# Kernel tuning notes

Measured on AMD Instinct MI355X. Metric: run time of the kernel, lower is better.

The kernel has to match this reference:

```python
import jax, jax.numpy as jnp
import numpy as np


def setup_inputs() -> dict:
    key = jax.random.key(0)
    kx, kw = jax.random.split(key)
    x = jax.random.normal(kx, (32, 256, 56, 56), dtype=jnp.float32)
    weight = jax.random.uniform(kw, (256, 256, 3, 3), dtype=jnp.float32) * 0.001
    return {"x": x, "weight": weight}


def reference(x, weight):
    # --- binarize activations with straight-through estimator ---
    # forward value = sign(x); gradient flows through clamp(x, -1, 1)
    clipped_x = jnp.clip(x, -1.0, 1.0)
    bx = jax.lax.stop_gradient(jnp.sign(x) - clipped_x) + clipped_x

    # --- binarize weights (per-output-channel mean-centered, scaled sign) ---
    w = weight
    # subtract per-output-channel mean over (in_c, kh, kw)
    bw = w - jnp.mean(w.reshape(w.shape[0], -1), axis=-1)[:, None, None, None]
    # per-output-channel scaling factor = mean |bw| (detached)
    scale = jnp.mean(jnp.abs(bw), axis=(1, 2, 3), keepdims=True)
    scale = jax.lax.stop_gradient(scale)
    clipped_w = jnp.clip(bw, -1.0, 1.0)
    binary_w = jax.lax.stop_gradient(scale * jnp.sign(bw) - clipped_w) + clipped_w

    # --- conv2d, NCHW / OIHW, stride 1, padding 1 ---
    y = jax.lax.conv_general_dilated(
        bx, binary_w,
        window_strides=(1, 1),
        padding=((1, 1), (1, 1)),
        dimension_numbers=("NCHW", "OIHW", "NCHW"),
    )
    return y
```

## Files before the change

### kernel.cpp

```cpp
#include <hip/hip_runtime.h>
#include <cstdint>
#include <cstddef>

#define N_ 32
#define C_ 256
#define H_ 56
#define W_ 56

typedef int v4i __attribute__((ext_vector_type(4)));

static constexpr size_t SX_BYTES = (size_t)N_ * 58 * 68 * 256;
static constexpr size_t WB_OFF   = SX_BYTES;
static constexpr size_t WB_BYTES = 36ull * 16 * 64 * 16;
static constexpr size_t SC_OFF   = WB_OFF + WB_BYTES;

__global__ __launch_bounds__(256) void zero_sx(v4i* __restrict__ p) {
    size_t i = (size_t)blockIdx.x * 256 + threadIdx.x;
    v4i z = {0, 0, 0, 0};
    p[i] = z;
}

__global__ __launch_bounds__(256) void pack_x(const float* __restrict__ x,
                                              char* __restrict__ sx) {
    __shared__ float tile[64 * 65];
    int tid = threadIdx.x;
    int hw0 = blockIdx.x * 64;
    int cb0 = blockIdx.y;
    int n   = blockIdx.z;

    int cl = tid >> 6, hwl = tid & 63;
    const float* xb = x + ((size_t)n * C_ + cb0 * 64) * 3136 + hw0;
#pragma unroll
    for (int i = 0; i < 16; ++i) {
        int cloc = i * 4 + cl;
        tile[cloc * 65 + hwl] = xb[(size_t)cloc * 3136 + hwl];
    }
    __syncthreads();

    int hwl2 = tid >> 2, cq = tid & 3;
    int hw = hw0 + hwl2;
    int h = hw / 56, w = hw - h * 56;
    int words[4];
#pragma unroll
    for (int g = 0; g < 4; ++g) {
        int word = 0;
#pragma unroll
        for (int b = 0; b < 4; ++b) {
            float v = tile[(cq * 16 + g * 4 + b) * 65 + hwl2];
            int s = (v > 0.0f) - (v < 0.0f);
            word |= (s & 0xff) << (8 * b);
        }
        words[g] = word;
    }
    v4i o4 = {words[0], words[1], words[2], words[3]};
    *(v4i*)(sx + (((size_t)n * 58 + h + 1) * 68 + (w + 1)) * 256 + cb0 * 64 + cq * 16) = o4;
}

__global__ __launch_bounds__(256) void pack_w(const float* __restrict__ wt,
                                              char* __restrict__ wB,
                                              float* __restrict__ scaleg) {
    __shared__ double red[256];
    int o = blockIdx.x, tid = threadIdx.x;
    const float* wo = wt + (size_t)o * 2304;

    double s = 0;
    for (int j = tid; j < 2304; j += 256) s += (double)wo[j];
    red[tid] = s;
    __syncthreads();
    for (int k = 128; k > 0; k >>= 1) {
        if (tid < k) red[tid] += red[tid + k];
        __syncthreads();
    }
    double mean = red[0] / 2304.0;
    __syncthreads();

    double s2 = 0;
    for (int j = tid; j < 2304; j += 256) s2 += fabs((double)wo[j] - mean);
    red[tid] = s2;
    __syncthreads();
    for (int k = 128; k > 0; k >>= 1) {
        if (tid < k) red[tid] += red[tid + k];
        __syncthreads();
    }
    if (tid == 0) scaleg[o] = (float)(red[0] / 2304.0);

    if (tid < 144) {
        int kiter = tid >> 2, q = tid & 3;
        int tap = kiter >> 2, cb = kiter & 3;
        int kh = tap / 3, kw = tap - kh * 3;
        int words[4];
        for (int g = 0; g < 4; ++g) {
            int word = 0;
            for (int b = 0; b < 4; ++b) {
                int c = cb * 64 + q * 16 + g * 4 + b;
                double v = (double)wo[c * 9 + kh * 3 + kw];
                int sg = (v > mean) - (v < mean);
                word |= (sg & 0xff) << (8 * b);
            }
            words[g] = word;
        }
        v4i pk = {words[0], words[1], words[2], words[3]};
        *(v4i*)(wB + (((size_t)kiter * 16 + (o >> 4)) * 64 + q * 16 + (o & 15)) * 16) = pk;
    }
}

__global__ __launch_bounds__(256, 3) void conv_mfma(const char* __restrict__ sx,
                                                    const v4i* __restrict__ wB,
                                                    const float* __restrict__ scaleg,
                                                    float* __restrict__ out) {
    __shared__ char xs[3 * 68 * 256];
    int tid = threadIdx.x;
    int wave = tid >> 6, lane = tid & 63;
    int h = blockIdx.x, n = blockIdx.y;

    const char* src = sx + ((size_t)n * 58 + h) * (68 * 256);
    for (int i = tid; i < 3 * 68 * 16; i += 256) {
        int w = (i >> 4) % 68;
        v4i v = *(const v4i*)(src + (size_t)i * 16);
        int phys = (i & ~15) | ((i + w) & 15);
        *(v4i*)(xs + (size_t)phys * 16) = v;
    }
    __syncthreads();

    int lm = lane & 15, q = lane >> 4;
    v4i acc[4][4];
#pragma unroll
    for (int mf = 0; mf < 4; ++mf)
#pragma unroll
        for (int of = 0; of < 4; ++of) {
            v4i z = {0, 0, 0, 0};
            acc[mf][of] = z;
        }

    for (int dh = 0; dh < 3; ++dh)
        for (int dw = 0; dw < 3; ++dw)
            for (int cb = 0; cb < 4; ++cb) {
                int kiter = (dh * 3 + dw) * 4 + cb;
                v4i b[4];
#pragma unroll
                for (int of = 0; of < 4; ++of)
                    b[of] = wB[((size_t)kiter * 16 + wave * 4 + of) * 64 + lane];
                v4i a[4];
#pragma unroll
                for (int mf = 0; mf < 4; ++mf) {
                    int win = mf * 16 + lm + dw;
                    int phys = ((dh * 68 + win) << 4) | ((cb * 4 + q + win) & 15);
                    a[mf] = *(const v4i*)(xs + (size_t)phys * 16);
                }
#pragma unroll
                for (int mf = 0; mf < 4; ++mf)
#pragma unroll
                    for (int of = 0; of < 4; ++of)
                        acc[mf][of] = __builtin_amdgcn_mfma_i32_16x16x64_i8(
                            a[mf], b[of], acc[mf][of], 0, 0, 0);
            }

#pragma unroll
    for (int of = 0; of < 4; ++of) {
        int o = (wave * 4 + of) * 16 + lm;
        float s = scaleg[o];
        float* ob = out + ((size_t)(n * C_ + o) * H_ + h) * W_;
#pragma unroll
        for (int mf = 0; mf < 4; ++mf) {
            int wb = mf * 16 + q * 4;
            if (wb < W_) {
                float4 v = {s * (float)acc[mf][of].x, s * (float)acc[mf][of].y,
                            s * (float)acc[mf][of].z, s * (float)acc[mf][of].w};
                *(float4*)(ob + wb) = v;
            }
        }
    }
}

extern "C" void kernel_launch(void* const* d_in, const int* in_sizes, int n_in,
                              void* d_out, int out_size, void* d_ws, size_t ws_size,
                              hipStream_t stream) {
    const float* x   = (const float*)d_in[0];
    const float* wgt = (const float*)d_in[1];
    float* out = (float*)d_out;
    char* ws = (char*)d_ws;

    char*  sx = ws;
    char*  wb = ws + WB_OFF;
    float* sg = (float*)(ws + SC_OFF);

    zero_sx<<<dim3(7888), dim3(256), 0, stream>>>((v4i*)sx);
    pack_x<<<dim3(49, 4, N_), dim3(256), 0, stream>>>(x, sx);
    pack_w<<<dim3(256), dim3(256), 0, stream>>>(wgt, wb, sg);
    conv_mfma<<<dim3(H_, N_), dim3(256), 0, stream>>>(sx, (const v4i*)wb, sg, out);
}
```

Before: 276.4 us.

## Compute two output rows per block, zero only halo, pre-swizzle packed input

The conv kernel now handles two output rows per block, 112 pixels in 7 MFMA M-fragments instead of 4 fragments with padding waste. This reuses each weight fragment load across more MFMAs and cuts the number of blocks. It double-buffers A/B fragment loads across k-iterations and lowers occupancy to 2 blocks per CU to make room for the larger accumulator set. The input zeroing is reduced to halo cells only, and pack_x now writes the bank-swizzled layout directly so the conv staging loop becomes a plain copy.

Result: faster. 248.2 us (-10.2%).

```diff
diff --git a/kernel.cpp b/kernel.cpp
--- a/kernel.cpp
+++ b/kernel.cpp
@@ -14,46 +14,72 @@
 static constexpr size_t WB_BYTES = 36ull * 16 * 64 * 16;
 static constexpr size_t SC_OFF   = WB_OFF + WB_BYTES;
 
-__global__ __launch_bounds__(256) void zero_sx(v4i* __restrict__ p) {
-    size_t i = (size_t)blockIdx.x * 256 + threadIdx.x;
+__global__ __launch_bounds__(256) void zero_halo(char* __restrict__ sx) {
+    int row = blockIdx.x;
+    int n   = blockIdx.y;
     v4i z = {0, 0, 0, 0};
-    p[i] = z;
+    char* base = sx + ((size_t)n * 58 + row) * (68 * 256);
+    if (row == 0 || row == 57) {
+        for (int i = threadIdx.x; i < 58 * 16; i += 256)
+            *(v4i*)(base + (size_t)i * 16) = z;
+    } else {
+        int tid = threadIdx.x;
+        if (tid < 32) {
+            int wpos = (tid >> 4) * 57;
+            int ch   = tid & 15;
+            *(v4i*)(base + ((size_t)wpos * 16 + ch) * 16) = z;
+        }
+    }
 }
 
 __global__ __launch_bounds__(256) void pack_x(const float* __restrict__ x,
                                               char* __restrict__ sx) {
     __shared__ float tile[64 * 65];
+    __shared__ char  ob[64 * 256];
     int tid = threadIdx.x;
     int hw0 = blockIdx.x * 64;
-    int cb0 = blockIdx.y;
-    int n   = blockIdx.z;
-
-    int cl = tid >> 6, hwl = tid & 63;
-    const float* xb = x + ((size_t)n * C_ + cb0 * 64) * 3136 + hw0;
-#pragma unroll
-    for (int i = 0; i < 16; ++i) {
-        int cloc = i * 4 + cl;
-        tile[cloc * 65 + hwl] = xb[(size_t)cloc * 3136 + hwl];
-    }
-    __syncthreads();
-
-    int hwl2 = tid >> 2, cq = tid & 3;
-    int hw = hw0 + hwl2;
-    int h = hw / 56, w = hw - h * 56;
-    int words[4];
-#pragma unroll
-    for (int g = 0; g < 4; ++g) {
-        int word = 0;
-#pragma unroll
-        for (int b = 0; b < 4; ++b) {
-            float v = tile[(cq * 16 + g * 4 + b) * 65 + hwl2];
-            int s = (v > 0.0f) - (v < 0.0f);
-            word |= (s & 0xff) << (8 * b);
-        }
-        words[g] = word;
-    }
-    v4i o4 = {words[0], words[1], words[2], words[3]};
-    *(v4i*)(sx + (((size_t)n * 58 + h + 1) * 68 + (w + 1)) * 256 + cb0 * 64 + cq * 16) = o4;
+    int n   = blockIdx.y;
+
+    int cl   = tid >> 6, hwl = tid & 63;
+    int hwl2 = tid >> 2, cq  = tid & 3;
+
+    for (int cb = 0; cb < 4; ++cb) {
+        const float* xb = x + ((size_t)n * C_ + cb * 64) * 3136 + hw0;
+#pragma unroll
+        for (int i = 0; i < 16; ++i) {
+            int cloc = i * 4 + cl;
+            tile[cloc * 65 + hwl] = xb[(size_t)cloc * 3136 + hwl];
+        }
+        __syncthreads();
+        int words[4];
+#pragma unroll
+        for (int g = 0; g < 4; ++g) {
+            int word = 0;
+#pragma unroll
+            for (int b = 0; b < 4; ++b) {
+                float v = tile[(cq * 16 + g * 4 + b) * 65 + hwl2];
+                int s = (v > 0.0f) - (v < 0.0f);
+                word |= (s & 0xff) << (8 * b);
+            }
+            words[g] = word;
+        }
+        v4i o4 = {words[0], words[1], words[2], words[3]};
+        int ch   = cb * 4 + cq;
+        int slot = (ch + hwl2) & 15;
+        *(v4i*)(ob + hwl2 * 256 + slot * 16) = o4;
+        __syncthreads();
+    }
+
+#pragma unroll
+    for (int j = 0; j < 4; ++j) {
+        int i = tid + j * 256;
+        int hwl3 = i >> 4, ch = i & 15;
+        v4i v = *(const v4i*)(ob + hwl3 * 256 + ((ch + hwl3) & 15) * 16);
+        int hw = hw0 + hwl3;
+        int h = hw / 56, w = hw - h * 56;
+        int slot = (ch + (w + 1)) & 15;
+        *(v4i*)(sx + (((size_t)n * 58 + h + 1) * 68 + (w + 1)) * 256 + slot * 16) = v;
+    }
 }
 
 __global__ __launch_bounds__(256) void pack_w(const float* __restrict__ wt,
@@ -104,70 +130,119 @@
     }
 }
 
-__global__ __launch_bounds__(256, 3) void conv_mfma(const char* __restrict__ sx,
+__global__ __launch_bounds__(256, 2) void conv_mfma(const char* __restrict__ sx,
                                                     const v4i* __restrict__ wB,
                                                     const float* __restrict__ scaleg,
                                                     float* __restrict__ out) {
-    __shared__ char xs[3 * 68 * 256];
+    __shared__ char xs[4 * 58 * 256];
     int tid = threadIdx.x;
     int wave = tid >> 6, lane = tid & 63;
-    int h = blockIdx.x, n = blockIdx.y;
-
-    const char* src = sx + ((size_t)n * 58 + h) * (68 * 256);
-    for (int i = tid; i < 3 * 68 * 16; i += 256) {
-        int w = (i >> 4) % 68;
-        v4i v = *(const v4i*)(src + (size_t)i * 16);
-        int phys = (i & ~15) | ((i + w) & 15);
-        *(v4i*)(xs + (size_t)phys * 16) = v;
-    }
-    __syncthreads();
+    int hp = blockIdx.x, n = blockIdx.y;
+    int h0 = hp * 2;
+
+    const char* src = sx + ((size_t)n * 58 + h0) * (68 * 256);
+    for (int i = tid; i < 4 * 58 * 16; i += 256) {
+        int pos = i >> 4;
+        int row = pos / 58;
+        int w   = pos - row * 58;
+        v4i v = *(const v4i*)(src + ((size_t)(row * 68 + w) << 8) + ((size_t)(i & 15) << 4));
+        *(v4i*)(xs + (size_t)i * 16) = v;
+    }
 
     int lm = lane & 15, q = lane >> 4;
-    v4i acc[4][4];
-#pragma unroll
-    for (int mf = 0; mf < 4; ++mf)
-#pragma unroll
-        for (int of = 0; of < 4; ++of) {
-            v4i z = {0, 0, 0, 0};
-            acc[mf][of] = z;
-        }
-
-    for (int dh = 0; dh < 3; ++dh)
-        for (int dw = 0; dw < 3; ++dw)
-            for (int cb = 0; cb < 4; ++cb) {
-                int kiter = (dh * 3 + dw) * 4 + cb;
-                v4i b[4];
-#pragma unroll
-                for (int of = 0; of < 4; ++of)
-                    b[of] = wB[((size_t)kiter * 16 + wave * 4 + of) * 64 + lane];
-                v4i a[4];
-#pragma unroll
-                for (int mf = 0; mf < 4; ++mf) {
-                    int win = mf * 16 + lm + dw;
-                    int phys = ((dh * 68 + win) << 4) | ((cb * 4 + q + win) & 15);
-                    a[mf] = *(const v4i*)(xs + (size_t)phys * 16);
-                }
-#pragma unroll
-                for (int mf = 0; mf < 4; ++mf)
-#pragma unroll
-                    for (int of = 0; of < 4; ++of)
-                        acc[mf][of] = __builtin_amdgcn_mfma_i32_16x16x64_i8(
-                            a[mf], b[of], acc[mf][of], 0, 0, 0);
-            }
+
+    int wof[7], ro[7];
+#pragma unroll
+    for (int mf = 0; mf < 7; ++mf) {
+        int m = mf * 16 + lm;
+        int r = (m >= 56) ? 1 : 0;
+        ro[mf]  = r;
+        wof[mf] = m - 56 * r;
+    }
+
+    v4i acc[7][4];
+#pragma unroll
+    for (int mf = 0; mf < 7; ++mf)
+#pragma unroll
+        for (int of = 0; of < 4; ++of) { v4i z = {0, 0, 0, 0}; acc[mf][of] = z; }
+
+    const v4i* wBw = wB + (size_t)(wave * 4) * 64 + lane;
+
+    __syncthreads();
+
+    v4i bA[4], bB[4], aA[7], aB[7];
+
+#pragma unroll
+    for (int of = 0; of < 4; ++of) bA[of] = wBw[of * 64];
+    {
+        int cbq = q;
+#pragma unroll
+        for (int mf = 0; mf < 7; ++mf) {
+            int win  = wof[mf];
+            int pos  = ro[mf] * 58 + win;
+            int phys = (pos << 4) | ((cbq + win) & 15);
+            aA[mf] = *(const v4i*)(xs + ((size_t)phys << 4));
+        }
+    }
+
+    for (int k2 = 0; k2 < 18; ++k2) {
+        int k0 = 2 * k2, k1 = k0 + 1;
+#pragma unroll
+        for (int of = 0; of < 4; ++of) bB[of] = wBw[(size_t)k1 * 1024 + of * 64];
+        {
+            int tap = k1 >> 2, cb = k1 & 3;
+            int dh = tap / 3, dw = tap - dh * 3;
+            int cbq = cb * 4 + q;
+#pragma unroll
+            for (int mf = 0; mf < 7; ++mf) {
+                int win  = wof[mf] + dw;
+                int pos  = (dh + ro[mf]) * 58 + win;
+                int phys = (pos << 4) | ((cbq + win) & 15);
+                aB[mf] = *(const v4i*)(xs + ((size_t)phys << 4));
+            }
+        }
+#pragma unroll
+        for (int mf = 0; mf < 7; ++mf)
+#pragma unroll
+            for (int of = 0; of < 4; ++of)
+                acc[mf][of] = __builtin_amdgcn_mfma_i32_16x16x64_i8(
+                    aA[mf], bA[of], acc[mf][of], 0, 0, 0);
+        if (k2 < 17) {
+            int kn = k0 + 2;
+#pragma unroll
+            for (int of = 0; of < 4; ++of) bA[of] = wBw[(size_t)kn * 1024 + of * 64];
+            int tap = kn >> 2, cb = kn & 3;
+            int dh = tap / 3, dw = tap - dh * 3;
+            int cbq = cb * 4 + q;
+#pragma unroll
+            for (int mf = 0; mf < 7; ++mf) {
+                int win  = wof[mf] + dw;
+                int pos  = (dh + ro[mf]) * 58 + win;
+                int phys = (pos << 4) | ((cbq + win) & 15);
+                aA[mf] = *(const v4i*)(xs + ((size_t)phys << 4));
+            }
+        }
+#pragma unroll
+        for (int mf = 0; mf < 7; ++mf)
+#pragma unroll
+            for (int of = 0; of < 4; ++of)
+                acc[mf][of] = __builtin_amdgcn_mfma_i32_16x16x64_i8(
+                    aB[mf], bB[of], acc[mf][of], 0, 0, 0);
+    }
 
 #pragma unroll
     for (int of = 0; of < 4; ++of) {
         int o = (wave * 4 + of) * 16 + lm;
         float s = scaleg[o];
-        float* ob = out + ((size_t)(n * C_ + o) * H_ + h) * W_;
-#pragma unroll
-        for (int mf = 0; mf < 4; ++mf) {
-            int wb = mf * 16 + q * 4;
-            if (wb < W_) {
-                float4 v = {s * (float)acc[mf][of].x, s * (float)acc[mf][of].y,
-                            s * (float)acc[mf][of].z, s * (float)acc[mf][of].w};
-                *(float4*)(ob + wb) = v;
-            }
+#pragma unroll
+        for (int mf = 0; mf < 7; ++mf) {
+            int m  = mf * 16 + q * 4;
+            int r  = (m >= 56) ? 1 : 0;
+            int wb = m - 56 * r;
+            float* ob = out + ((size_t)(n * C_ + o) * H_ + h0 + r) * W_ + wb;
+            float4 v = {s * (float)acc[mf][of].x, s * (float)acc[mf][of].y,
+                        s * (float)acc[mf][of].z, s * (float)acc[mf][of].w};
+            *(float4*)ob = v;
         }
     }
 }
@@ -184,8 +259,8 @@
     char*  wb = ws + WB_OFF;
     float* sg = (float*)(ws + SC_OFF);
 
-    zero_sx<<<dim3(7888), dim3(256), 0, stream>>>((v4i*)sx);
-    pack_x<<<dim3(49, 4, N_), dim3(256), 0, stream>>>(x, sx);
+    zero_halo<<<dim3(58, N_), dim3(256), 0, stream>>>(sx);
+    pack_x<<<dim3(49, N_), dim3(256), 0, stream>>>(x, sx);
     pack_w<<<dim3(256), dim3(256), 0, stream>>>(wgt, wb, sg);
-    conv_mfma<<<dim3(H_, N_), dim3(256), 0, stream>>>(sx, (const v4i*)wb, sg, out);
-}
+    conv_mfma<<<dim3(28, N_), dim3(256), 0, stream>>>(sx, (const v4i*)wb, sg, out);
+}
```
